# Kernel tuning notes

Hardware: AMD Instinct MI355X
Metric: run time of the kernel (lower is better)

Reference implementation:

```python
import jax, jax.numpy as jnp
import numpy as np

N_QUBITS = 12
N_LAYERS = 4
N_ACTIONS = 6
BATCH = 4096
DIM = 2 ** N_QUBITS


def _apply_1q(state, U, wire):
    """Apply a single-qubit gate on `wire` (PennyLane: wire 0 = most significant bit).
    state: (B, DIM) complex64; U: (2,2) or (B,2,2) complex64."""
    B = state.shape[0]
    left = 2 ** wire
    right = 2 ** (N_QUBITS - wire - 1)
    s = state.reshape(B, left, 2, right)
    if U.ndim == 3:
        s = jnp.einsum('bji,blir->bljr', U, s)  # per-sample gate (input encoding)
    else:
        s = jnp.einsum('ji,blir->bljr', U, s)   # shared gate (trainable weights)
    return s.reshape(B, DIM)


def _bit(idx, wire):
    # bit of basis index `idx` corresponding to `wire` (wire 0 = MSB)
    return (idx >> (N_QUBITS - 1 - wire)) & 1


def _rot_matrix(phi, theta, omega):
    # PennyLane Rot(phi, theta, omega) = RZ(omega) @ RY(theta) @ RZ(phi)
    ct = jnp.cos(theta * 0.5)
    st = jnp.sin(theta * 0.5)
    u00 = jnp.exp(-0.5j * (phi + omega)) * ct
    u01 = -jnp.exp(0.5j * (phi - omega)) * st
    u10 = jnp.exp(-0.5j * (phi - omega)) * st
    u11 = jnp.exp(0.5j * (phi + omega)) * ct
    return jnp.stack([jnp.stack([u00, u01]), jnp.stack([u10, u11])]).astype(jnp.complex64)


def setup_inputs() -> dict:
    key = jax.random.key(0)
    k1, k2, k3, k4 = jax.random.split(key, 4)
    x = jax.random.normal(k1, (BATCH, N_QUBITS), dtype=jnp.float32)
    # TorchLayer default init: uniform(0, 2*pi)
    weights = jax.random.uniform(k2, (N_LAYERS, N_QUBITS, 3), dtype=jnp.float32,
                                 minval=0.0, maxval=2.0 * np.pi)
    bound = 1.0 / np.sqrt(N_QUBITS)
    fc_w = jax.random.uniform(k3, (N_ACTIONS, N_QUBITS), dtype=jnp.float32,
                              minval=-bound, maxval=bound)
    fc_b = jax.random.uniform(k4, (N_ACTIONS,), dtype=jnp.float32,
                              minval=-bound, maxval=bound)
    return {"x": x, "weights": weights, "fc_w": fc_w, "fc_b": fc_b}


def reference(x, weights, fc_w, fc_b):
    B = x.shape[0]
    # |0...0> initial state, batched
    state = jnp.zeros((B, DIM), dtype=jnp.complex64).at[:, 0].set(1.0)

    # Input encoding: RY(x[:, q]) on each wire q (per-sample gates)
    c = jnp.cos(0.5 * x)  # (B, nq)
    s = jnp.sin(0.5 * x)
    for q in range(N_QUBITS):
        cq, sq = c[:, q], s[:, q]
        U = jnp.stack([jnp.stack([cq, -sq], axis=-1),
                       jnp.stack([sq, cq], axis=-1)], axis=-2).astype(jnp.complex64)  # (B,2,2)
        state = _apply_1q(state, U, q)

    # CZ chain is diagonal; combined sign per basis state (same every layer)
    idx = jnp.arange(DIM)
    cz_sign = jnp.ones((DIM,), dtype=jnp.float32)
    for q in range(N_QUBITS - 1):
        both = (_bit(idx, q) & _bit(idx, q + 1)).astype(jnp.float32)
        cz_sign = cz_sign * (1.0 - 2.0 * both)
    cz_diag = cz_sign.astype(jnp.complex64)

    # Variational layers: Rot on each wire, then CZ chain
    for l in range(N_LAYERS):
        for q in range(N_QUBITS):
            U = _rot_matrix(weights[l, q, 0], weights[l, q, 1], weights[l, q, 2])
            state = _apply_1q(state, U, q)
        state = state * cz_diag[None, :]

    # <Z_q> = sum_i |amp_i|^2 * (1 - 2*bit_q(i))
    probs = state.real ** 2 + state.imag ** 2  # (B, DIM) float32
    zmat = jnp.stack([1.0 - 2.0 * _bit(idx, q).astype(jnp.float32)
                      for q in range(N_QUBITS)], axis=-1)  # (DIM, nq)
    q_out = probs @ zmat  # (B, nq)

    return q_out @ fc_w.T + fc_b
```

## Files before the change

### kernel.cpp

```cpp
#include <hip/hip_runtime.h>
#include <math.h>

#define NQ 12
#define NL 4
#define NA 6
#define BATCH 4096
#define NT 256
#define RSTR 17

typedef float f2 __attribute__((ext_vector_type(2)));

#define CMUL(d, u, a)  asm("v_pk_mul_f32 %0, %1, %2 op_sel_hi:[0,1]"                 : "=v"(d) : "v"(u), "v"(a))
#define CMACR(d, u, a) asm("v_pk_fma_f32 %0, %1, %2, %0 op_sel_hi:[0,1,1]"           : "+v"(d) : "v"(u), "v"(a))
#define CMACI(d, u, a) asm("v_pk_fma_f32 %0, %1, %2, %0 op_sel:[1,1,0] op_sel_hi:[1,0,1] neg_lo:[1,0,0]" : "+v"(d) : "v"(u), "v"(a))
#define RYMULS(d, u, a)  asm("v_pk_mul_f32 %0, %1, %2 op_sel:[1,0] op_sel_hi:[1,1]"  : "=v"(d) : "v"(u), "v"(a))
#define RYMACNS(d, u, a) asm("v_pk_fma_f32 %0, %1, %2, %0 op_sel:[1,0,0] op_sel_hi:[1,1,1] neg_lo:[1,0,0] neg_hi:[1,0,0]" : "+v"(d) : "v"(u), "v"(a))
#define WFENCE() asm volatile("s_waitcnt lgkmcnt(0)" ::: "memory")

#define RYBFLY(A0, A1, CS) do { \
    f2 _a0 = (A0), _a1 = (A1), _n0, _n1; \
    CMUL  (_n0, CS, _a0); RYMACNS(_n0, CS, _a1); \
    RYMULS(_n1, CS, _a0); CMACR  (_n1, CS, _a1); \
    (A0) = _n0; (A1) = _n1; } while (0)

#define RYGATE(gidx, bq) do { \
    const f2 cs = *(const f2*)(rots + (gidx) * 2); \
    const int S = 1 << (bq); \
    _Pragma("unroll") \
    for (int m = 0; m < 8; ++m) { \
        const int j0 = ((m & ~(S - 1)) << 1) | (m & (S - 1)); \
        RYBFLY(st[j0], st[j0 + S], cs); \
    } } while (0)


__global__ void setup_kernel(const float* __restrict__ weights, float* __restrict__ ws) {
    const int t = threadIdx.x;
    if (t < NL * NQ) {
        const float th = weights[t * 3 + 1];
        float s, c;
        sincosf(0.5f * th, &s, &c);
        ws[t * 2 + 0] = c; ws[t * 2 + 1] = s;
        const int r = t / NQ, q = t % NQ;
        float a;
        if (r == 0) a = 0.5f * weights[q * 3 + 0];
        else        a = 0.5f * (weights[((r - 1) * NQ + q) * 3 + 2] +
                                 weights[(r * NQ + q) * 3 + 0]);
        ws[96 + t] = a;
    }
    {
        const int d = t >> 4, j = t & 15;
        int wq[4];
        if (d == 1 || d == 3) { wq[0] = 0; wq[1] = 1; wq[2] = 6; wq[3] = 7; }
        else                  { wq[0] = 8; wq[1] = 9; wq[2] = 10; wq[3] = 11; }
        float g = 0.0f;
#pragma unroll
        for (int k = 0; k < 4; ++k) {
            const int q = wq[k];
            const float a = (d == 0) ? 0.5f * weights[q * 3 + 0]
                                     : 0.5f * (weights[((d - 1) * NQ + q) * 3 + 2] +
                                               weights[(d * NQ + q) * 3 + 0]);
            g += ((j >> (3 - k)) & 1) ? a : -a;
        }
        float sg, cg;
        sincosf(g, &sg, &cg);
        ws[144 + (d * 16 + j) * 2 + 0] = cg;
        ws[144 + (d * 16 + j) * 2 + 1] = sg;
    }
}

__device__ __forceinline__ void apply_phase(f2* st, const float* tab, float beta) {
    float sb, cb;
    sincosf(beta, &sb, &cb);
    const f2 Dth = (f2){cb, sb};
#pragma unroll
    for (int j = 0; j < 16; ++j) {
        const f2 a = st[j];
        f2 t, u;
        CMUL(t, Dth, a); CMACI(t, Dth, a);
        const f2 dg = *(const f2*)(tab + 2 * j);
        CMUL(u, dg, t); CMACI(u, dg, t);
        st[j] = u;
    }
}

__global__ __launch_bounds__(NT) void qdqn_kernel(
    const float* __restrict__ x,
    const float* __restrict__ rots,
    const float* __restrict__ fc_w,
    const float* __restrict__ fc_b,
    float* __restrict__ out)
{
    __shared__ __align__(16) f2 buf[NT * RSTR];
    __shared__ float encc[NQ], encs[NQ];
    __shared__ float red[4][NQ];
    __shared__ float qout[NQ];

    const int tix = threadIdx.x;
    const int lam = tix & 63;
    const int w   = tix >> 6;
    const int w1  = (w >> 1) & 1, w0 = w & 1;
    const int b   = blockIdx.x;

    const float* alph = rots + 96;
    const float* dreg = rots + 144;

    if (tix < NQ) {
        float s, c;
        sincosf(0.5f * x[b * NQ + tix], &s, &c);
        encc[tix] = c; encs[tix] = s;
    }
    __syncthreads();

    f2 st[16];
    {
        float pre = 1.0f;
#pragma unroll
        for (int q = 0; q < 6; ++q)
            pre *= ((lam >> (5 - q)) & 1) ? encs[q] : encc[q];
        pre *= w1 ? encs[6] : encc[6];
        pre *= w0 ? encs[7] : encc[7];
        const float c8 = encc[8],  s8 = encs[8];
        const float c9 = encc[9],  s9 = encs[9];
        const float cA = encc[10], sA = encs[10];
        const float cB = encc[11], sB = encs[11];
#pragma unroll
        for (int j = 0; j < 16; ++j) {
            float v = pre;
            v *= (j & 8) ? s8 : c8;
            v *= (j & 4) ? s9 : c9;
            v *= (j & 2) ? sA : cA;
            v *= (j & 1) ? sB : cB;
            st[j] = (f2){ v, 0.0f };
        }
    }

#define BETA_L1(al) ( (((lam >> 5) & 1) ? (al)[0] : -(al)[0]) + (((lam >> 4) & 1) ? (al)[1] : -(al)[1]) \
                    + (((lam >> 3) & 1) ? (al)[2] : -(al)[2]) + (((lam >> 2) & 1) ? (al)[3] : -(al)[3]) \
                    + (((lam >> 1) & 1) ? (al)[4] : -(al)[4]) + (((lam >> 0) & 1) ? (al)[5] : -(al)[5]) \
                    + (w1 ? (al)[6] : -(al)[6]) + (w0 ? (al)[7] : -(al)[7]) )
#define BETA_L3(al) ( (((lam >> 5) & 1) ? (al)[2] : -(al)[2]) + (((lam >> 4) & 1) ? (al)[3] : -(al)[3]) \
                    + (w1 ? (al)[4] : -(al)[4]) + (w0 ? (al)[5] : -(al)[5]) \
                    + (((lam >> 3) & 1) ? (al)[8] : -(al)[8]) + (((lam >> 2) & 1) ? (al)[9] : -(al)[9]) \
                    + (((lam >> 1) & 1) ? (al)[10] : -(al)[10]) + (((lam >> 0) & 1) ? (al)[11] : -(al)[11]) )

    apply_phase(st, dreg + 0 * 32, BETA_L1(alph + 0 * NQ));

    const int col_b = ((lam >> 4) << 2) | w;
    const int row_a = (w << 6) | (lam & 0x30);
    const int col_a = lam & 0xF;

#define TRANSPOSE_A_FWD() do { \
    WFENCE(); \
    _Pragma("unroll") for (int j = 0; j < 16; ++j) buf[tix * RSTR + j] = st[j]; \
    WFENCE(); \
    _Pragma("unroll") for (int j = 0; j < 16; ++j) st[j] = buf[(row_a | j) * RSTR + col_a]; \
    } while (0)

#define TB_READ(j) buf[(((j & 3) << 6) | ((j >> 2) << 4) | (lam & 0xF)) * RSTR + col_b]

#pragma unroll 1
    for (int h = 0; h < 2; ++h) {
        {
            const int gb = (2 * h) * NQ;
            RYGATE(gb + 11, 0); RYGATE(gb + 10, 1); RYGATE(gb + 9, 2); RYGATE(gb + 8, 3);
            TRANSPOSE_A_FWD();
            RYGATE(gb + 5, 0); RYGATE(gb + 4, 1); RYGATE(gb + 3, 2); RYGATE(gb + 2, 3);
            WFENCE();
#pragma unroll
            for (int j = 0; j < 16; ++j) buf[tix * RSTR + j] = st[j];
            __syncthreads();
#pragma unroll
            for (int j = 0; j < 16; ++j) st[j] = TB_READ(j);
            RYGATE(gb + 7, 0); RYGATE(gb + 6, 1); RYGATE(gb + 1, 2); RYGATE(gb + 0, 3);
            {
                const int l5 = (lam >> 5) & 1, l4 = (lam >> 4) & 1, l3 = (lam >> 3) & 1;
                const int par = (l5 & l4) + (l4 & w1) + (w1 & w0) + __popc(lam & (lam >> 1) & 0x7);
                const float base = (par & 1) ? -1.0f : 1.0f;
                const float fA = l5 ? -1.0f : 1.0f;
                const float fB = w0 ? -1.0f : 1.0f;
                const float fC = l3 ? -1.0f : 1.0f;
#pragma unroll
                for (int j = 0; j < 16; ++j) {
                    float s = base;
                    if (j & 4) s *= fA;
                    if (j & 2) s *= fB;
                    if (j & 1) s *= fC;
                    if ((((j & 12) == 12) ? 1 : 0) ^ (((j & 3) == 3) ? 1 : 0)) s = -s;
                    st[j] *= s;
                }
            }
            apply_phase(st, dreg + (2 * h + 1) * 32, BETA_L3(alph + (2 * h + 1) * NQ));
        }
        {
            const int gb = (2 * h + 1) * NQ;
            RYGATE(gb + 7, 0); RYGATE(gb + 6, 1); RYGATE(gb + 1, 2); RYGATE(gb + 0, 3);
            __syncthreads();
#pragma unroll
            for (int j = 0; j < 16; ++j) buf[tix * RSTR + j] = st[j];
            __syncthreads();
#pragma unroll
            for (int j = 0; j < 16; ++j) st[j] = TB_READ(j);
            RYGATE(gb + 5, 0); RYGATE(gb + 4, 1); RYGATE(gb + 3, 2); RYGATE(gb + 2, 3);
            __syncthreads();
#pragma unroll
            for (int j = 0; j < 16; ++j) buf[tix * RSTR + j] = st[j];
            WFENCE();
#pragma unroll
            for (int j = 0; j < 16; ++j) st[j] = buf[(row_a | j) * RSTR + col_a];
            RYGATE(gb + 11, 0); RYGATE(gb + 10, 1); RYGATE(gb + 9, 2); RYGATE(gb + 8, 3);
            if (h == 0) {
                {
                    const int par = __popc(lam & (lam >> 1)) + ((lam & 1) & w1) + (w1 & w0);
                    const float base = (par & 1) ? -1.0f : 1.0f;
                    const float sHi = w0 ? -base : base;
#pragma unroll
                    for (int j = 0; j < 16; ++j) {
                        float s = (j & 8) ? sHi : base;
                        if (__popc(j & (j >> 1)) & 1) s = -s;
                        st[j] *= s;
                    }
                }
                apply_phase(st, dreg + 2 * 32, BETA_L1(alph + 2 * NQ));
            }
        }
    }

    float tot = 0.f, m8 = 0.f, m9 = 0.f, m10 = 0.f, m11 = 0.f;
#pragma unroll
    for (int j = 0; j < 16; ++j) {
        const float p = st[j].x * st[j].x + st[j].y * st[j].y;
        tot += p;
        m8  += (j & 8) ? -p : p;
        m9  += (j & 4) ? -p : p;
        m10 += (j & 2) ? -p : p;
        m11 += (j & 1) ? -p : p;
    }
    float part[NQ];
#pragma unroll
    for (int q = 0; q < 6; ++q)
        part[q] = ((lam >> (5 - q)) & 1) ? -tot : tot;
    part[6] = w1 ? -tot : tot;
    part[7] = w0 ? -tot : tot;
    part[8] = m8; part[9] = m9; part[10] = m10; part[11] = m11;

#pragma unroll
    for (int off = 32; off > 0; off >>= 1) {
#pragma unroll
        for (int q = 0; q < NQ; ++q)
            part[q] += __shfl_down(part[q], off, 64);
    }
    if (lam == 0) {
#pragma unroll
        for (int q = 0; q < NQ; ++q) red[w][q] = part[q];
    }
    __syncthreads();
    if (tix < NQ) qout[tix] = red[0][tix] + red[1][tix] + red[2][tix] + red[3][tix];
    __syncthreads();

    if (tix < NA) {
        float acc = fc_b[tix];
#pragma unroll
        for (int q = 0; q < NQ; ++q)
            acc += qout[q] * fc_w[tix * NQ + q];
        out[b * NA + tix] = acc;
    }
}

extern "C" void kernel_launch(void* const* d_in, const int* in_sizes, int n_in,
                              void* d_out, int out_size, void* d_ws, size_t ws_size,
                              hipStream_t stream) {
    const float* x   = (const float*)d_in[0];
    const float* wts = (const float*)d_in[1];
    const float* fcw = (const float*)d_in[2];
    const float* fcb = (const float*)d_in[3];
    float* tabs = (float*)d_ws;
    setup_kernel<<<1, 64, 0, stream>>>(wts, tabs);
    qdqn_kernel<<<BATCH, NT, 0, stream>>>(x, tabs, fcw, fcb, (float*)d_out);
}
```

Baseline: 146.8 us.

## Process two batch samples per block to amortize gate coefficient loads

Each block now simulates two samples' state vectors (stA, stB) at once and launches half as many blocks. Gate coefficients, phase tables and sign factors are loaded once and applied to both states, which gives more independent instructions per thread for ILP. In exchange the register count doubles, which may lower occupancy or cause spills. The shared transpose buffer is reused serially for the two states, so extra barriers are added.

```diff
diff --git a/kernel.cpp b/kernel.cpp
--- a/kernel.cpp
+++ b/kernel.cpp
@@ -6,6 +6,7 @@
 #define NA 6
 #define BATCH 4096
 #define NT 256
+#define NBLK (BATCH / 2)
 #define RSTR 17
 
 typedef float f2 __attribute__((ext_vector_type(2)));
@@ -23,13 +24,14 @@
     RYMULS(_n1, CS, _a0); CMACR  (_n1, CS, _a1); \
     (A0) = _n0; (A1) = _n1; } while (0)
 
-#define RYGATE(gidx, bq) do { \
+#define RYGATE2(gidx, bq) do { \
     const f2 cs = *(const f2*)(rots + (gidx) * 2); \
     const int S = 1 << (bq); \
     _Pragma("unroll") \
     for (int m = 0; m < 8; ++m) { \
         const int j0 = ((m & ~(S - 1)) << 1) | (m & (S - 1)); \
-        RYBFLY(st[j0], st[j0 + S], cs); \
+        RYBFLY(stA[j0], stA[j0 + S], cs); \
+        RYBFLY(stB[j0], stB[j0 + S], cs); \
     } } while (0)
 
 
@@ -68,21 +70,6 @@
     }
 }
 
-__device__ __forceinline__ void apply_phase(f2* st, const float* tab, float beta) {
-    float sb, cb;
-    sincosf(beta, &sb, &cb);
-    const f2 Dth = (f2){cb, sb};
-#pragma unroll
-    for (int j = 0; j < 16; ++j) {
-        const f2 a = st[j];
-        f2 t, u;
-        CMUL(t, Dth, a); CMACI(t, Dth, a);
-        const f2 dg = *(const f2*)(tab + 2 * j);
-        CMUL(u, dg, t); CMACI(u, dg, t);
-        st[j] = u;
-    }
-}
-
 __global__ __launch_bounds__(NT) void qdqn_kernel(
     const float* __restrict__ x,
     const float* __restrict__ rots,
@@ -91,38 +78,43 @@
     float* __restrict__ out)
 {
     __shared__ __align__(16) f2 buf[NT * RSTR];
-    __shared__ float encc[NQ], encs[NQ];
-    __shared__ float red[4][NQ];
-    __shared__ float qout[NQ];
+    __shared__ float encc[2][NQ], encs[2][NQ];
+    __shared__ float redA[4][NQ], redB[4][NQ];
+    __shared__ float qoutA[NQ], qoutB[NQ];
 
     const int tix = threadIdx.x;
     const int lam = tix & 63;
     const int w   = tix >> 6;
     const int w1  = (w >> 1) & 1, w0 = w & 1;
-    const int b   = blockIdx.x;
+    const int b0  = blockIdx.x * 2;
 
     const float* alph = rots + 96;
     const float* dreg = rots + 144;
 
-    if (tix < NQ) {
-        float s, c;
-        sincosf(0.5f * x[b * NQ + tix], &s, &c);
-        encc[tix] = c; encs[tix] = s;
+    if (tix < 2 * NQ) {
+        const int s = tix / NQ, q = tix % NQ;
+        float sn, cs;
+        sincosf(0.5f * x[(b0 + s) * NQ + q], &sn, &cs);
+        encc[s][q] = cs; encs[s][q] = sn;
     }
     __syncthreads();
 
-    f2 st[16];
-    {
+    f2 stA[16], stB[16];
+#pragma unroll
+    for (int s = 0; s < 2; ++s) {
+        const float* ec = encc[s];
+        const float* es = encs[s];
         float pre = 1.0f;
 #pragma unroll
         for (int q = 0; q < 6; ++q)
-            pre *= ((lam >> (5 - q)) & 1) ? encs[q] : encc[q];
-        pre *= w1 ? encs[6] : encc[6];
-        pre *= w0 ? encs[7] : encc[7];
-        const float c8 = encc[8],  s8 = encs[8];
-        const float c9 = encc[9],  s9 = encs[9];
-        const float cA = encc[10], sA = encs[10];
-        const float cB = encc[11], sB = encs[11];
+            pre *= ((lam >> (5 - q)) & 1) ? es[q] : ec[q];
+        pre *= w1 ? es[6] : ec[6];
+        pre *= w0 ? es[7] : ec[7];
+        const float c8 = ec[8],  s8 = es[8];
+        const float c9 = ec[9],  s9 = es[9];
+        const float cA = ec[10], sA = es[10];
+        const float cB = ec[11], sB = es[11];
+        f2* st = s ? stB : stA;
 #pragma unroll
         for (int j = 0; j < 16; ++j) {
             float v = pre;
@@ -143,35 +135,56 @@
                     + (((lam >> 3) & 1) ? (al)[8] : -(al)[8]) + (((lam >> 2) & 1) ? (al)[9] : -(al)[9]) \
                     + (((lam >> 1) & 1) ? (al)[10] : -(al)[10]) + (((lam >> 0) & 1) ? (al)[11] : -(al)[11]) )
 
-    apply_phase(st, dreg + 0 * 32, BETA_L1(alph + 0 * NQ));
+#define APPLY_PHASE2(tab, beta) do { \
+    float _sb, _cb; \
+    sincosf((beta), &_sb, &_cb); \
+    const f2 _Dth = (f2){_cb, _sb}; \
+    _Pragma("unroll") \
+    for (int j = 0; j < 16; ++j) { \
+        const f2 _dg = *(const f2*)((tab) + 2 * j); \
+        f2 _t, _u; \
+        CMUL(_t, _Dth, stA[j]); CMACI(_t, _Dth, stA[j]); \
+        CMUL(_u, _dg, _t);      CMACI(_u, _dg, _t); \
+        stA[j] = _u; \
+        CMUL(_t, _Dth, stB[j]); CMACI(_t, _Dth, stB[j]); \
+        CMUL(_u, _dg, _t);      CMACI(_u, _dg, _t); \
+        stB[j] = _u; \
+    } } while (0)
+
+    APPLY_PHASE2(dreg + 0 * 32, BETA_L1(alph + 0 * NQ));
 
     const int col_b = ((lam >> 4) << 2) | w;
     const int row_a = (w << 6) | (lam & 0x30);
     const int col_a = lam & 0xF;
 
-#define TRANSPOSE_A_FWD() do { \
+#define TA_PASS(ST) do { \
     WFENCE(); \
-    _Pragma("unroll") for (int j = 0; j < 16; ++j) buf[tix * RSTR + j] = st[j]; \
+    _Pragma("unroll") for (int j = 0; j < 16; ++j) buf[tix * RSTR + j] = ST[j]; \
     WFENCE(); \
-    _Pragma("unroll") for (int j = 0; j < 16; ++j) st[j] = buf[(row_a | j) * RSTR + col_a]; \
+    _Pragma("unroll") for (int j = 0; j < 16; ++j) ST[j] = buf[(row_a | j) * RSTR + col_a]; \
     } while (0)
 
-#define TB_READ(j) buf[(((j & 3) << 6) | ((j >> 2) << 4) | (lam & 0xF)) * RSTR + col_b]
+#define TB_WRITE(ST) { _Pragma("unroll") for (int j = 0; j < 16; ++j) buf[tix * RSTR + j] = ST[j]; }
+#define TB_READ_ST(ST) { _Pragma("unroll") for (int j = 0; j < 16; ++j) \
+        ST[j] = buf[(((j & 3) << 6) | ((j >> 2) << 4) | (lam & 0xF)) * RSTR + col_b]; }
 
 #pragma unroll 1
     for (int h = 0; h < 2; ++h) {
         {
             const int gb = (2 * h) * NQ;
-            RYGATE(gb + 11, 0); RYGATE(gb + 10, 1); RYGATE(gb + 9, 2); RYGATE(gb + 8, 3);
-            TRANSPOSE_A_FWD();
-            RYGATE(gb + 5, 0); RYGATE(gb + 4, 1); RYGATE(gb + 3, 2); RYGATE(gb + 2, 3);
+            RYGATE2(gb + 11, 0); RYGATE2(gb + 10, 1); RYGATE2(gb + 9, 2); RYGATE2(gb + 8, 3);
+            TA_PASS(stA);
+            TA_PASS(stB);
+            RYGATE2(gb + 5, 0); RYGATE2(gb + 4, 1); RYGATE2(gb + 3, 2); RYGATE2(gb + 2, 3);
             WFENCE();
-#pragma unroll
-            for (int j = 0; j < 16; ++j) buf[tix * RSTR + j] = st[j];
-            __syncthreads();
-#pragma unroll
-            for (int j = 0; j < 16; ++j) st[j] = TB_READ(j);
-            RYGATE(gb + 7, 0); RYGATE(gb + 6, 1); RYGATE(gb + 1, 2); RYGATE(gb + 0, 3);
+            TB_WRITE(stA);
+            __syncthreads();
+            TB_READ_ST(stA);
+            __syncthreads();
+            TB_WRITE(stB);
+            __syncthreads();
+            TB_READ_ST(stB);
+            RYGATE2(gb + 7, 0); RYGATE2(gb + 6, 1); RYGATE2(gb + 1, 2); RYGATE2(gb + 0, 3);
             {
                 const int l5 = (lam >> 5) & 1, l4 = (lam >> 4) & 1, l3 = (lam >> 3) & 1;
                 const int par = (l5 & l4) + (l4 & w1) + (w1 & w0) + __popc(lam & (lam >> 1) & 0x7);
@@ -186,28 +199,28 @@
                     if (j & 2) s *= fB;
                     if (j & 1) s *= fC;
                     if ((((j & 12) == 12) ? 1 : 0) ^ (((j & 3) == 3) ? 1 : 0)) s = -s;
-                    st[j] *= s;
+                    stA[j] *= s;
+                    stB[j] *= s;
                 }
             }
-            apply_phase(st, dreg + (2 * h + 1) * 32, BETA_L3(alph + (2 * h + 1) * NQ));
+            APPLY_PHASE2(dreg + (2 * h + 1) * 32, BETA_L3(alph + (2 * h + 1) * NQ));
         }
         {
             const int gb = (2 * h + 1) * NQ;
-            RYGATE(gb + 7, 0); RYGATE(gb + 6, 1); RYGATE(gb + 1, 2); RYGATE(gb + 0, 3);
-            __syncthreads();
-#pragma unroll
-            for (int j = 0; j < 16; ++j) buf[tix * RSTR + j] = st[j];
-            __syncthreads();
-#pragma unroll
-            for (int j = 0; j < 16; ++j) st[j] = TB_READ(j);
-            RYGATE(gb + 5, 0); RYGATE(gb + 4, 1); RYGATE(gb + 3, 2); RYGATE(gb + 2, 3);
-            __syncthreads();
-#pragma unroll
-            for (int j = 0; j < 16; ++j) buf[tix * RSTR + j] = st[j];
-            WFENCE();
-#pragma unroll
-            for (int j = 0; j < 16; ++j) st[j] = buf[(row_a | j) * RSTR + col_a];
-            RYGATE(gb + 11, 0); RYGATE(gb + 10, 1); RYGATE(gb + 9, 2); RYGATE(gb + 8, 3);
+            RYGATE2(gb + 7, 0); RYGATE2(gb + 6, 1); RYGATE2(gb + 1, 2); RYGATE2(gb + 0, 3);
+            __syncthreads();
+            TB_WRITE(stA);
+            __syncthreads();
+            TB_READ_ST(stA);
+            __syncthreads();
+            TB_WRITE(stB);
+            __syncthreads();
+            TB_READ_ST(stB);
+            RYGATE2(gb + 5, 0); RYGATE2(gb + 4, 1); RYGATE2(gb + 3, 2); RYGATE2(gb + 2, 3);
+            __syncthreads();
+            TA_PASS(stA);
+            TA_PASS(stB);
+            RYGATE2(gb + 11, 0); RYGATE2(gb + 10, 1); RYGATE2(gb + 9, 2); RYGATE2(gb + 8, 3);
             if (h == 0) {
                 {
                     const int par = __popc(lam & (lam >> 1)) + ((lam & 1) & w1) + (w1 & w0);
@@ -217,52 +230,68 @@
                     for (int j = 0; j < 16; ++j) {
                         float s = (j & 8) ? sHi : base;
                         if (__popc(j & (j >> 1)) & 1) s = -s;
-                        st[j] *= s;
+                        stA[j] *= s;
+                        stB[j] *= s;
                     }
                 }
-                apply_phase(st, dreg + 2 * 32, BETA_L1(alph + 2 * NQ));
+                APPLY_PHASE2(dreg + 2 * 32, BETA_L1(alph + 2 * NQ));
             }
         }
     }
 
-    float tot = 0.f, m8 = 0.f, m9 = 0.f, m10 = 0.f, m11 = 0.f;
+    float totA = 0.f, a8 = 0.f, a9 = 0.f, a10 = 0.f, a11 = 0.f;
+    float totB = 0.f, b8 = 0.f, b9 = 0.f, b10 = 0.f, b11 = 0.f;
 #pragma unroll
     for (int j = 0; j < 16; ++j) {
-        const float p = st[j].x * st[j].x + st[j].y * st[j].y;
-        tot += p;
-        m8  += (j & 8) ? -p : p;
-        m9  += (j & 4) ? -p : p;
-        m10 += (j & 2) ? -p : p;
-        m11 += (j & 1) ? -p : p;
-    }
-    float part[NQ];
-#pragma unroll
-    for (int q = 0; q < 6; ++q)
-        part[q] = ((lam >> (5 - q)) & 1) ? -tot : tot;
-    part[6] = w1 ? -tot : tot;
-    part[7] = w0 ? -tot : tot;
-    part[8] = m8; part[9] = m9; part[10] = m10; part[11] = m11;
+        const float pA = stA[j].x * stA[j].x + stA[j].y * stA[j].y;
+        const float pB = stB[j].x * stB[j].x + stB[j].y * stB[j].y;
+        totA += pA; totB += pB;
+        a8  += (j & 8) ? -pA : pA;  b8  += (j & 8) ? -pB : pB;
+        a9  += (j & 4) ? -pA : pA;  b9  += (j & 4) ? -pB : pB;
+        a10 += (j & 2) ? -pA : pA;  b10 += (j & 2) ? -pB : pB;
+        a11 += (j & 1) ? -pA : pA;  b11 += (j & 1) ? -pB : pB;
+    }
+    float pA[NQ], pB[NQ];
+#pragma unroll
+    for (int q = 0; q < 6; ++q) {
+        const int bit = (lam >> (5 - q)) & 1;
+        pA[q] = bit ? -totA : totA;
+        pB[q] = bit ? -totB : totB;
+    }
+    pA[6] = w1 ? -totA : totA;  pB[6] = w1 ? -totB : totB;
+    pA[7] = w0 ? -totA : totA;  pB[7] = w0 ? -totB : totB;
+    pA[8] = a8; pA[9] = a9; pA[10] = a10; pA[11] = a11;
+    pB[8] = b8; pB[9] = b9; pB[10] = b10; pB[11] = b11;
 
 #pragma unroll
     for (int off = 32; off > 0; off >>= 1) {
 #pragma unroll
-        for (int q = 0; q < NQ; ++q)
-            part[q] += __shfl_down(part[q], off, 64);
+        for (int q = 0; q < NQ; ++q) {
+            pA[q] += __shfl_down(pA[q], off, 64);
+            pB[q] += __shfl_down(pB[q], off, 64);
+        }
     }
     if (lam == 0) {
 #pragma unroll
-        for (int q = 0; q < NQ; ++q) red[w][q] = part[q];
+        for (int q = 0; q < NQ; ++q) { redA[w][q] = pA[q]; redB[w][q] = pB[q]; }
     }
     __syncthreads();
-    if (tix < NQ) qout[tix] = red[0][tix] + red[1][tix] + red[2][tix] + red[3][tix];
+    if (tix < NQ) {
+        qoutA[tix] = redA[0][tix] + redA[1][tix] + redA[2][tix] + redA[3][tix];
+        qoutB[tix] = redB[0][tix] + redB[1][tix] + redB[2][tix] + redB[3][tix];
+    }
     __syncthreads();
 
     if (tix < NA) {
-        float acc = fc_b[tix];
-#pragma unroll
-        for (int q = 0; q < NQ; ++q)
-            acc += qout[q] * fc_w[tix * NQ + q];
-        out[b * NA + tix] = acc;
+        float accA = fc_b[tix], accB = accA;
+#pragma unroll
+        for (int q = 0; q < NQ; ++q) {
+            const float f = fc_w[tix * NQ + q];
+            accA += qoutA[q] * f;
+            accB += qoutB[q] * f;
+        }
+        out[b0 * NA + tix] = accA;
+        out[(b0 + 1) * NA + tix] = accB;
     }
 }
 
@@ -275,5 +304,5 @@
     const float* fcb = (const float*)d_in[3];
     float* tabs = (float*)d_ws;
     setup_kernel<<<1, 64, 0, stream>>>(wts, tabs);
-    qdqn_kernel<<<BATCH, NT, 0, stream>>>(x, tabs, fcw, fcb, (float*)d_out);
+    qdqn_kernel<<<NBLK, NT, 0, stream>>>(x, tabs, fcw, fcb, (float*)d_out);
 }
```

New measurement: 149.9 us. +2.1%, slower.
